# Performance work log

Measured on AMD Instinct MI355X. Metric: run time of the kernel, lower is better.

## Reference

```python
import jax, jax.numpy as jnp
import numpy as np

# Grids: sparse_shape=(41,320,320); after spcv1 stride(2,1,1) pad1 k3 -> (21,320,320);
# after spcv2 stride(2,1,1) pad(0,1,1) k3 -> (10,320,320); after spcv3 k(3,1,1) stride(2,1,1) -> (4,320,320)
GRID0 = (41, 320, 320)
GRID1 = (21, 320, 320)
GRID2 = (10, 320, 320)
GRID3 = (4, 320, 320)
T = 3
C_IN = 16
BN_EPS = 1e-3


def _idx_grid(coords, shape):
    g = -np.ones(shape, np.int32)
    g[coords[:, 0], coords[:, 1], coords[:, 2]] = np.arange(len(coords), dtype=np.int32)
    return g


def _subm_nbrs(coords, grid):
    M = len(coords)
    nbr = -np.ones((M, 27), np.int32)
    sh = np.array(grid.shape)
    k = 0
    for dz in (-1, 0, 1):
        for dy in (-1, 0, 1):
            for dx in (-1, 0, 1):
                c = coords + np.array([dz, dy, dx])
                ok = np.all((c >= 0) & (c < sh), axis=1)
                nbr[ok, k] = grid[c[ok, 0], c[ok, 1], c[ok, 2]]
                k += 1
    return nbr


def _spconv_pairs(coords_in, grid_in, out_shape, ksz, stride, pad):
    ksz = np.array(ksz); st = np.array(stride); pd = np.array(pad); osh = np.array(out_shape)
    cands = []
    for kz in range(ksz[0]):
        for ky in range(ksz[1]):
            for kx in range(ksz[2]):
                o = coords_in + pd - np.array([kz, ky, kx])
                ok = np.all(o % st == 0, axis=1)
                o = o[ok] // st
                ok2 = np.all((o >= 0) & (o < osh), axis=1)
                cands.append(o[ok2])
    coords_out = np.unique(np.concatenate(cands, 0), axis=0)
    M = len(coords_out); K = int(np.prod(ksz))
    idx = -np.ones((M, K), np.int32)
    sh = np.array(grid_in.shape)
    k = 0
    for kz in range(ksz[0]):
        for ky in range(ksz[1]):
            for kx in range(ksz[2]):
                ci = coords_out * st - pd + np.array([kz, ky, kx])
                ok = np.all((ci >= 0) & (ci < sh), axis=1)
                idx[ok, k] = grid_in[ci[ok, 0], ci[ok, 1], ci[ok, 2]]
                k += 1
    return coords_out.astype(np.int32), idx


def setup_inputs() -> dict:
    rng = np.random.default_rng(0)
    # clustered lidar-like active voxels
    nC, nP = 60, 150
    centers = np.stack([rng.uniform(6, 35, nC), rng.uniform(12, 308, nC), rng.uniform(12, 308, nC)], 1)
    pts = centers[:, None, :] + rng.normal(size=(nC, nP, 3)) * np.array([1.2, 2.0, 2.0])
    pts = np.clip(np.round(pts).astype(np.int64).reshape(-1, 3), 0, np.array(GRID0) - 1)
    coords0 = np.unique(pts, axis=0)
    g0 = _idx_grid(coords0, GRID0)
    nbr0 = _subm_nbrs(coords0, g0)
    coords1, idx1 = _spconv_pairs(coords0, g0, GRID1, (3, 3, 3), (2, 1, 1), (1, 1, 1))
    g1 = _idx_grid(coords1, GRID1)
    nbr1 = _subm_nbrs(coords1, g1)
    coords2, idx2 = _spconv_pairs(coords1, g1, GRID2, (3, 3, 3), (2, 1, 1), (0, 1, 1))
    g2 = _idx_grid(coords2, GRID2)
    nbr2 = _subm_nbrs(coords2, g2)
    coords3, idx3 = _spconv_pairs(coords2, g2, GRID3, (3, 1, 1), (2, 1, 1), (0, 0, 0))

    def w(K, ci, co):
        return jnp.asarray(rng.standard_normal((K, ci, co)) / np.sqrt(K * ci), jnp.float32)

    def bn(n, c):
        g = rng.uniform(0.5, 1.5, (n, c)); b = rng.standard_normal((n, c)) * 0.1
        m = rng.standard_normal((n, c)) * 0.1; v = rng.uniform(0.5, 1.5, (n, c))
        return jnp.asarray(np.stack([g, b, m, v], 1), jnp.float32)  # [n,4,c]

    return dict(
        voxel_features=jnp.asarray(rng.standard_normal((T, len(coords0), C_IN)), jnp.float32),
        w_subm1=w(27, 16, 32), w_subm2=w(27, 32, 32), w_spcv1=w(27, 32, 64),
        w_subm3=w(27, 64, 64), w_subm4=w(27, 64, 64), w_subm5=w(27, 64, 64),
        w_spcv2=w(27, 64, 64), w_subm6=w(27, 64, 64), w_subm7=w(27, 64, 64), w_subm8=w(27, 64, 64),
        w_spcv3=w(3, 64, 64),
        w_ad1=jnp.asarray(rng.standard_normal((64, 64)) / 8.0, jnp.float32),
        w_ad2=jnp.asarray(rng.standard_normal((64, 64)) / 8.0, jnp.float32),
        bn32=bn(2, 32), bn64=bn(9, 64), bn_ad=bn(1, 64)[0],
        nbr0=jnp.asarray(nbr0), idx1=jnp.asarray(idx1), nbr1=jnp.asarray(nbr1),
        idx2=jnp.asarray(idx2), nbr2=jnp.asarray(nbr2), idx3=jnp.asarray(idx3),
        coords3=jnp.asarray(coords3))


def _bn_eval(x, p):
    g, b, m, v = p
    return (x - m) * (g * jax.lax.rsqrt(v + BN_EPS)) + b


def _gconv(f, idx, w):
    # gather-GEMM: idx [M,K] (-1 = missing), f [Min,Ci], w [K,Ci,Co]
    g = jnp.where((idx >= 0)[:, :, None], f[jnp.clip(idx, 0)], 0.0)  # [M,K,Ci]
    return jnp.einsum('mki,kio->mo', g, w)


def reference(voxel_features, w_subm1, w_subm2, w_spcv1, w_subm3, w_subm4, w_subm5,
              w_spcv2, w_subm6, w_subm7, w_subm8, w_spcv3, w_ad1, w_ad2,
              bn32, bn64, bn_ad, nbr0, idx1, nbr1, idx2, nbr2, idx3, coords3):
    relu = jax.nn.relu
    s0 = s1 = s2 = None  # cached previous-frame sparse features per level
    outs = []
    for t in range(voxel_features.shape[0]):
        a0 = 0.0 if s0 is None else jnp.mean(s0, 0)
        a1 = 0.0 if s1 is None else jnp.mean(s1, 0)
        a2 = 0.0 if s2 is None else jnp.mean(s2, 0)
        x = relu(_bn_eval(_gconv(voxel_features[t], nbr0, w_subm1), bn32[0]))
        x = relu(_bn_eval(_gconv(x, nbr0, w_subm2), bn32[1]))
        x3 = relu(_bn_eval(_gconv(x, idx1, w_spcv1) + a0, bn64[0])); s0 = x3
        x = relu(_bn_eval(_gconv(x3, nbr1, w_subm3), bn64[1]))
        x = relu(_bn_eval(_gconv(x, nbr1, w_subm4), bn64[2]))
        x6 = relu(_bn_eval(_gconv(x, nbr1, w_subm5), bn64[3]))
        x7 = relu(_bn_eval(_gconv(x6, idx2, w_spcv2) + a1, bn64[4])); s1 = x7
        x = relu(_bn_eval(_gconv(x7, nbr2, w_subm6), bn64[5]))
        x = relu(_bn_eval(_gconv(x, nbr2, w_subm7), bn64[6]))
        x10 = relu(_bn_eval(_gconv(x, nbr2, w_subm8), bn64[7]))
        x11 = relu(_bn_eval(_gconv(x10, idx3, w_spcv3) + a2, bn64[8])); s2 = x11
        dense = jnp.zeros(GRID3 + (64,), x11.dtype).at[coords3[:, 0], coords3[:, 1], coords3[:, 2]].set(x11)
        outs.append(dense.transpose(3, 0, 1, 2).reshape(1, 64 * GRID3[0], GRID3[1], GRID3[2]))
        adapt = lambda s: (relu(_bn_eval(s @ w_ad1, bn_ad)) @ w_ad2) / 10.0
        s0, s1, s2 = adapt(s0), adapt(s1), adapt(s2)
    return jnp.stack(outs)
```

## Files before the change

kernel.cpp:

```cpp
#include <hip/hip_runtime.h>


typedef _Float16 f16;
typedef _Float16 f16x8 __attribute__((ext_vector_type(8)));
typedef float    f32x4 __attribute__((ext_vector_type(4)));

#define BN_EPS_F 1e-3f

__global__ __launch_bounds__(256)
void fill_zero(float4* __restrict__ p, long n4)
{
    long i  = blockIdx.x * 256L + threadIdx.x;
    long st = (long)gridDim.x * 256L;
    float4 z = make_float4(0.f, 0.f, 0.f, 0.f);
    for (; i < n4; i += st) p[i] = z;
}

__global__ __launch_bounds__(256)
void vf_convert(const float* __restrict__ vf, f16* __restrict__ vf16, int nrows)
{
    int i = blockIdx.x * 256 + threadIdx.x;
    if (i >= nrows * 32) return;
    int r = i >> 5, c = i & 31;
    vf16[i] = (c < 16) ? (f16)vf[r * 16 + c] : (f16)0;
}

struct WXA { const float* s; f16* d; int K, Ci, Co, CiD, off; };
struct WXAll { WXA w[11]; };

__global__ __launch_bounds__(256)
void wxform_all(WXAll wa, int total)
{
    int i = blockIdx.x * 256 + threadIdx.x;
    if (i >= total) return;
    int j = 0;
    #pragma unroll
    for (int t = 1; t < 11; ++t) if (i >= wa.w[t].off) j = t;
    const float* s = wa.w[j].s;
    f16* d = wa.w[j].d;
    int Ci = wa.w[j].Ci, Co = wa.w[j].Co, CiD = wa.w[j].CiD;
    int e = i - wa.w[j].off;
    int cc = Co * CiD;
    int k = e / cc; int rem = e - k * cc;
    int co = rem / CiD; int ci = rem - co * CiD;
    float v = (ci < Ci) ? s[((size_t)k * Ci + ci) * Co + co] : 0.f;
    d[e] = (f16)v;
}

template<int Ci, int Co, int K, int ROWS, int KSPLIT, bool SCATTER>
__global__ __launch_bounds__((ROWS/16)*KSPLIT*64)
void gconv(const f16* __restrict__ fin, const int* __restrict__ idx,
           const f16* __restrict__ wT,
           const float* __restrict__ bnp,
           const float* __restrict__ avec,
           f16* __restrict__ fout,
           const int* __restrict__ coords, float* __restrict__ dout,
           int M, int blocksPerFrame, long finStride, long foutStride)
{
    constexpr int RW  = ROWS / 16;
    constexpr int NW  = RW * KSPLIT;
    constexpr int NT  = NW * 64;
    constexpr int NF  = Co / 16;
    constexpr int KK  = Ci / 32;
    constexpr int TPG = (K + KSPLIT - 1) / KSPLIT;
    constexpr int CoP = Co + 4;

    __shared__ int   sIdx[ROWS][K];
    __shared__ float red[KSPLIT > 1 ? KSPLIT - 1 : 1][ROWS][CoP];

    const int tid  = threadIdx.x;
    const int lane = tid & 63;
    const int w    = tid >> 6;
    const int wq   = w % RW;
    const int g    = w / RW;
    const int l15  = lane & 15;
    const int kg   = lane >> 4;

    const int bid   = blockIdx.x;
    const int frame = bid / blocksPerFrame;
    const int fb    = bid - frame * blocksPerFrame;
    const f16* finF = fin + (long)frame * finStride;
    f16* foutF      = fout + (long)frame * foutStride;
    const int m0    = fb * ROWS;

    for (int i = tid; i < ROWS * K; i += NT) {
        int r = i / K, k = i - r * K;
        int m = m0 + r;
        sIdx[r][k] = (m < M) ? idx[(long)m * K + k] : -1;
    }
    __syncthreads();

    f32x4 acc[NF];
    #pragma unroll
    for (int nf = 0; nf < NF; ++nf) acc[nf] = (f32x4){0.f, 0.f, 0.f, 0.f};

    const int arow = wq * 16 + l15;
    const int k0 = g * TPG;

    #pragma unroll
    for (int kt = 0; kt < TPG; ++kt) {
        int k = k0 + kt;
        if (k >= K) break;
        int n = sIdx[arow][k];
        #pragma unroll
        for (int kk = 0; kk < KK; ++kk) {
            f16x8 af = {};
            if (n >= 0)
                af = *(const f16x8*)&finF[(long)n * Ci + kk * 32 + kg * 8];
            #pragma unroll
            for (int nf = 0; nf < NF; ++nf) {
                f16x8 bf = *(const f16x8*)&wT[((long)k * Co + nf * 16 + l15) * Ci + kk * 32 + kg * 8];
                acc[nf] = __builtin_amdgcn_mfma_f32_16x16x32_f16(af, bf, acc[nf], 0, 0, 0);
            }
        }
    }

    if (KSPLIT > 1) {
        if (g > 0) {
            #pragma unroll
            for (int nf = 0; nf < NF; ++nf)
                #pragma unroll
                for (int j = 0; j < 4; ++j)
                    red[g - 1][wq * 16 + kg * 4 + j][nf * 16 + l15] = acc[nf][j];
        }
        __syncthreads();
        if (g == 0) {
            #pragma unroll
            for (int nf = 0; nf < NF; ++nf)
                #pragma unroll
                for (int j = 0; j < 4; ++j)
                    #pragma unroll
                    for (int gi = 0; gi < KSPLIT - 1; ++gi)
                        acc[nf][j] += red[gi][wq * 16 + kg * 4 + j][nf * 16 + l15];
        }
    }

    if (g == 0) {
        #pragma unroll
        for (int nf = 0; nf < NF; ++nf) {
            int c = nf * 16 + l15;
            float gg = bnp[c], bb = bnp[Co + c], mu = bnp[2 * Co + c], vv = bnp[3 * Co + c];
            float sc = gg * rsqrtf(vv + BN_EPS_F);
            float sh = bb - mu * sc;
            float av = avec ? avec[c] : 0.f;
            #pragma unroll
            for (int j = 0; j < 4; ++j) {
                int row = wq * 16 + kg * 4 + j;
                int m = m0 + row;
                if (m < M) {
                    float x = acc[nf][j] + av;
                    float y = fmaxf(fmaf(x, sc, sh), 0.f);
                    foutF[(long)m * Co + c] = (f16)y;
                    if (SCATTER) {
                        int z  = coords[m * 3 + 0];
                        int yy = coords[m * 3 + 1];
                        int xx = coords[m * 3 + 2];
                        dout[(long)(c * 4 + z) * (320 * 320) + yy * 320 + xx] = y;
                    }
                }
            }
        }
    }
}

__global__ __launch_bounds__(64)
void adapt_partial3(const f16* __restrict__ x3, const f16* __restrict__ x7,
                    const f16* __restrict__ x11,
                    const float* __restrict__ w_ad1, const float* __restrict__ bn_ad,
                    float* __restrict__ pb,
                    int M1, int M2, int M3, int g1, int g2)
{
    __shared__ float wl[64 * 64];
    const int c = threadIdx.x;
    for (int i = c; i < 64 * 64; i += 64) wl[i] = w_ad1[i];
    float gg = bn_ad[c], bb = bn_ad[64 + c], mu = bn_ad[128 + c], vv = bn_ad[192 + c];
    float sc = gg * rsqrtf(vv + BN_EPS_F);
    float sh = bb - mu * sc;
    __syncthreads();

    int b = blockIdx.x;
    const f16* s; int M, r0;
    if (b < g1)           { s = x3;  M = M1; r0 = b * 64; }
    else if (b < g1 + g2) { s = x7;  M = M2; r0 = (b - g1) * 64; }
    else                  { s = x11; M = M3; r0 = (b - g1 - g2) * 64; }

    float hacc = 0.f;
    int r1 = min(r0 + 64, M);
    for (int r = r0; r < r1; ++r) {
        float acc = 0.f;
        #pragma unroll
        for (int i8 = 0; i8 < 8; ++i8) {
            f16x8 sv = *(const f16x8*)&s[(size_t)r * 64 + i8 * 8];
            #pragma unroll
            for (int e = 0; e < 8; ++e)
                acc = fmaf((float)sv[e], wl[(i8 * 8 + e) * 64 + c], acc);
        }
        hacc += fmaxf(fmaf(acc, sc, sh), 0.f);
    }
    pb[(size_t)b * 64 + c] = hacc;
}

__global__ __launch_bounds__(192)
void adapt_final3(const float* __restrict__ pb, const float* __restrict__ w_ad2,
                  float* __restrict__ av, int g1, int g2, int g3,
                  float invM1, float invM2, float invM3)
{
    __shared__ float h[3][64];
    const int lvl = threadIdx.x >> 6;
    const int c   = threadIdx.x & 63;
    int base = (lvl == 0) ? 0 : (lvl == 1 ? g1 : g1 + g2);
    int n    = (lvl == 0) ? g1 : (lvl == 1 ? g2 : g3);
    float invM = (lvl == 0) ? invM1 : (lvl == 1 ? invM2 : invM3);
    float acc = 0.f;
    for (int i = 0; i < n; ++i) acc += pb[(size_t)(base + i) * 64 + c];
    h[lvl][c] = acc * invM;
    __syncthreads();
    float o = 0.f;
    #pragma unroll 8
    for (int j = 0; j < 64; ++j) o = fmaf(h[lvl][j], w_ad2[j * 64 + c], o);
    av[lvl * 64 + c] = o * 0.1f;
}

extern "C" void kernel_launch(void* const* d_in, const int* in_sizes, int n_in,
                              void* d_out, int out_size, void* d_ws, size_t ws_size,
                              hipStream_t stream)
{
    const float* vf      = (const float*)d_in[0];
    const float* w_subm1 = (const float*)d_in[1];
    const float* w_subm2 = (const float*)d_in[2];
    const float* w_spcv1 = (const float*)d_in[3];
    const float* w_subm3 = (const float*)d_in[4];
    const float* w_subm4 = (const float*)d_in[5];
    const float* w_subm5 = (const float*)d_in[6];
    const float* w_spcv2 = (const float*)d_in[7];
    const float* w_subm6 = (const float*)d_in[8];
    const float* w_subm7 = (const float*)d_in[9];
    const float* w_subm8 = (const float*)d_in[10];
    const float* w_spcv3 = (const float*)d_in[11];
    const float* w_ad1   = (const float*)d_in[12];
    const float* w_ad2   = (const float*)d_in[13];
    const float* bn32    = (const float*)d_in[14];
    const float* bn64    = (const float*)d_in[15];
    const float* bn_ad   = (const float*)d_in[16];
    const int* nbr0    = (const int*)d_in[17];
    const int* idx1    = (const int*)d_in[18];
    const int* nbr1    = (const int*)d_in[19];
    const int* idx2    = (const int*)d_in[20];
    const int* nbr2    = (const int*)d_in[21];
    const int* idx3    = (const int*)d_in[22];
    const int* coords3 = (const int*)d_in[23];

    const int M0 = in_sizes[0]  / (3 * 16);
    const int M1 = in_sizes[18] / 27;
    const int M2 = in_sizes[20] / 27;
    const int M3 = in_sizes[22] / 3;

    char* base = (char*)d_ws;
    size_t off = 0;
    auto alloc = [&](size_t bytes) -> void* {
        void* p = base + off;
        off = (off + bytes + 255) & ~(size_t)255;
        return p;
    };
    f16* wt1  = (f16*)alloc((size_t)27 * 32 * 32 * 2);
    f16* wt2  = (f16*)alloc((size_t)27 * 32 * 32 * 2);
    f16* wtc1 = (f16*)alloc((size_t)27 * 64 * 32 * 2);
    f16* wt3  = (f16*)alloc((size_t)27 * 64 * 64 * 2);
    f16* wt4  = (f16*)alloc((size_t)27 * 64 * 64 * 2);
    f16* wt5  = (f16*)alloc((size_t)27 * 64 * 64 * 2);
    f16* wtc2 = (f16*)alloc((size_t)27 * 64 * 64 * 2);
    f16* wt6  = (f16*)alloc((size_t)27 * 64 * 64 * 2);
    f16* wt7  = (f16*)alloc((size_t)27 * 64 * 64 * 2);
    f16* wt8  = (f16*)alloc((size_t)27 * 64 * 64 * 2);
    f16* wtc3 = (f16*)alloc((size_t)3  * 64 * 64 * 2);
    f16* vf16  = (f16*)alloc((size_t)3 * M0 * 32 * 2);
    f16* buf0a = (f16*)alloc((size_t)3 * M0 * 32 * 2);
    f16* buf0b = (f16*)alloc((size_t)3 * M0 * 32 * 2);
    f16* x3    = (f16*)alloc((size_t)M1 * 64 * 2);
    f16* buf1a = (f16*)alloc((size_t)M1 * 64 * 2);
    f16* buf1b = (f16*)alloc((size_t)M1 * 64 * 2);
    f16* x7    = (f16*)alloc((size_t)M2 * 64 * 2);
    f16* buf2a = (f16*)alloc((size_t)M2 * 64 * 2);
    f16* buf2b = (f16*)alloc((size_t)M2 * 64 * 2);
    f16* x11   = (f16*)alloc((size_t)M3 * 64 * 2);
    float* av  = (float*)alloc(192 * 4);
    const int g1a = (M1 + 63) / 64, g2a = (M2 + 63) / 64, g3a = (M3 + 63) / 64;
    float* pb  = (float*)alloc((size_t)(g1a + g2a + g3a) * 64 * 4);
    (void)ws_size; (void)n_in;

    WXAll wa;
    int woff = 0;
    auto addw = [&](int slot, const float* s, f16* d, int K, int Ci, int Co, int CiD) {
        wa.w[slot] = {s, d, K, Ci, Co, CiD, woff};
        woff += K * Co * CiD;
    };
    addw(0,  w_subm1, wt1,  27, 16, 32, 32);
    addw(1,  w_subm2, wt2,  27, 32, 32, 32);
    addw(2,  w_spcv1, wtc1, 27, 32, 64, 32);
    addw(3,  w_subm3, wt3,  27, 64, 64, 64);
    addw(4,  w_subm4, wt4,  27, 64, 64, 64);
    addw(5,  w_subm5, wt5,  27, 64, 64, 64);
    addw(6,  w_spcv2, wtc2, 27, 64, 64, 64);
    addw(7,  w_subm6, wt6,  27, 64, 64, 64);
    addw(8,  w_subm7, wt7,  27, 64, 64, 64);
    addw(9,  w_subm8, wt8,  27, 64, 64, 64);
    addw(10, w_spcv3, wtc3, 3,  64, 64, 64);
    wxform_all<<<(woff + 255) / 256, 256, 0, stream>>>(wa, woff);
    vf_convert<<<(3 * M0 * 32 + 255) / 256, 256, 0, stream>>>(vf, vf16, 3 * M0);
    fill_zero<<<2048, 256, 0, stream>>>((float4*)d_out, (long)out_size / 4);

    const int g0w = (M0 + 31) / 32;
    const int g1w = (M1 + 31) / 32;
    const int g2w = (M2 + 31) / 32;
    const int g3w = (M3 + 31) / 32;
    const long s0 = (long)M0 * 32;

    gconv<32,32,27,32,4,false><<<3 * g0w, 512, 0, stream>>>(
        vf16,  nbr0, wt1, bn32,       nullptr, buf0a, nullptr, nullptr, M0, g0w, s0, s0);
    gconv<32,32,27,32,4,false><<<3 * g0w, 512, 0, stream>>>(
        buf0a, nbr0, wt2, bn32 + 128, nullptr, buf0b, nullptr, nullptr, M0, g0w, s0, s0);

    for (int t = 0; t < 3; ++t) {
        const float* a0 = (t == 0) ? nullptr : av + 0;
        const float* a1 = (t == 0) ? nullptr : av + 64;
        const float* a2 = (t == 0) ? nullptr : av + 128;
        float* doutT = (float*)d_out + (size_t)t * 256 * 320 * 320;

        gconv<32,64,27,32,4,false><<<g1w, 512, 0, stream>>>(
            buf0b + (long)t * s0, idx1, wtc1, bn64, a0, x3, nullptr, nullptr, M1, g1w, 0, 0);
        gconv<64,64,27,32,4,false><<<g1w, 512, 0, stream>>>(
            x3,    nbr1, wt3, bn64 + 256,  nullptr, buf1a, nullptr, nullptr, M1, g1w, 0, 0);
        gconv<64,64,27,32,4,false><<<g1w, 512, 0, stream>>>(
            buf1a, nbr1, wt4, bn64 + 512,  nullptr, buf1b, nullptr, nullptr, M1, g1w, 0, 0);
        gconv<64,64,27,32,4,false><<<g1w, 512, 0, stream>>>(
            buf1b, nbr1, wt5, bn64 + 768,  nullptr, buf1a, nullptr, nullptr, M1, g1w, 0, 0);
        gconv<64,64,27,32,4,false><<<g2w, 512, 0, stream>>>(
            buf1a, idx2, wtc2, bn64 + 1024, a1,     x7,    nullptr, nullptr, M2, g2w, 0, 0);
        gconv<64,64,27,32,4,false><<<g2w, 512, 0, stream>>>(
            x7,    nbr2, wt6, bn64 + 1280, nullptr, buf2a, nullptr, nullptr, M2, g2w, 0, 0);
        gconv<64,64,27,32,4,false><<<g2w, 512, 0, stream>>>(
            buf2a, nbr2, wt7, bn64 + 1536, nullptr, buf2b, nullptr, nullptr, M2, g2w, 0, 0);
        gconv<64,64,27,32,4,false><<<g2w, 512, 0, stream>>>(
            buf2b, nbr2, wt8, bn64 + 1792, nullptr, buf2a, nullptr, nullptr, M2, g2w, 0, 0);
        gconv<64,64,3,32,3,true><<<g3w, 384, 0, stream>>>(
            buf2a, idx3, wtc3, bn64 + 2048, a2,    x11,   coords3, doutT,   M3, g3w, 0, 0);

        if (t < 2) {
            adapt_partial3<<<g1a + g2a + g3a, 64, 0, stream>>>(
                x3, x7, x11, w_ad1, bn_ad, pb, M1, M2, M3, g1a, g2a);
            adapt_final3<<<1, 192, 0, stream>>>(
                pb, w_ad2, av, g1a, g2a, g3a, 1.f / M1, 1.f / M2, 1.f / M3);
        }
    }
}
```

Before: 1.674 ms.

## Shrink gconv blocks to 16 rows with per-wave kernel-offset split

Restructures the gather-conv kernel so each block handles 16 output rows. Waves split the padded kernel offsets (27 padded to 28, 3 to 4), each wave taking a fixed number of taps. Neighbor indices are loaded straight into registers instead of staged through shared memory, and the split-K reduction is folded into the epilogue. Weights are zero-padded for the extra tap so the loops need no bounds checks. This doubles the block count, costs extra index loads and weight reads per row, and adds a wasted padded tap.

```diff
diff --git a/kernel.cpp b/kernel.cpp
--- a/kernel.cpp
+++ b/kernel.cpp
@@ -25,7 +25,7 @@
     vf16[i] = (c < 16) ? (f16)vf[r * 16 + c] : (f16)0;
 }
 
-struct WXA { const float* s; f16* d; int K, Ci, Co, CiD, off; };
+struct WXA { const float* s; f16* d; int K, Kp, Ci, Co, CiD, off; };
 struct WXAll { WXA w[11]; };
 
 __global__ __launch_bounds__(256)
@@ -38,17 +38,17 @@
     for (int t = 1; t < 11; ++t) if (i >= wa.w[t].off) j = t;
     const float* s = wa.w[j].s;
     f16* d = wa.w[j].d;
-    int Ci = wa.w[j].Ci, Co = wa.w[j].Co, CiD = wa.w[j].CiD;
+    int K = wa.w[j].K, Ci = wa.w[j].Ci, Co = wa.w[j].Co, CiD = wa.w[j].CiD;
     int e = i - wa.w[j].off;
     int cc = Co * CiD;
     int k = e / cc; int rem = e - k * cc;
     int co = rem / CiD; int ci = rem - co * CiD;
-    float v = (ci < Ci) ? s[((size_t)k * Ci + ci) * Co + co] : 0.f;
+    float v = (k < K && ci < Ci) ? s[((size_t)k * Ci + ci) * Co + co] : 0.f;
     d[e] = (f16)v;
 }
 
-template<int Ci, int Co, int K, int ROWS, int KSPLIT, bool SCATTER>
-__global__ __launch_bounds__((ROWS/16)*KSPLIT*64)
+template<int Ci, int Co, int K, int KPAD, int TPW, bool SCATTER>
+__global__ __launch_bounds__((KPAD/TPW)*64)
 void gconv(const f16* __restrict__ fin, const int* __restrict__ idx,
            const f16* __restrict__ wT,
            const float* __restrict__ bnp,
@@ -57,22 +57,16 @@
            const int* __restrict__ coords, float* __restrict__ dout,
            int M, int blocksPerFrame, long finStride, long foutStride)
 {
-    constexpr int RW  = ROWS / 16;
-    constexpr int NW  = RW * KSPLIT;
-    constexpr int NT  = NW * 64;
+    constexpr int KSPLIT = KPAD / TPW;
     constexpr int NF  = Co / 16;
     constexpr int KK  = Ci / 32;
-    constexpr int TPG = (K + KSPLIT - 1) / KSPLIT;
     constexpr int CoP = Co + 4;
 
-    __shared__ int   sIdx[ROWS][K];
-    __shared__ float red[KSPLIT > 1 ? KSPLIT - 1 : 1][ROWS][CoP];
+    __shared__ float red[KSPLIT - 1][16][CoP];
 
     const int tid  = threadIdx.x;
     const int lane = tid & 63;
-    const int w    = tid >> 6;
-    const int wq   = w % RW;
-    const int g    = w / RW;
+    const int g    = tid >> 6;
     const int l15  = lane & 15;
     const int kg   = lane >> 4;
 
@@ -81,27 +75,26 @@
     const int fb    = bid - frame * blocksPerFrame;
     const f16* finF = fin + (long)frame * finStride;
     f16* foutF      = fout + (long)frame * foutStride;
-    const int m0    = fb * ROWS;
-
-    for (int i = tid; i < ROWS * K; i += NT) {
-        int r = i / K, k = i - r * K;
-        int m = m0 + r;
-        sIdx[r][k] = (m < M) ? idx[(long)m * K + k] : -1;
-    }
-    __syncthreads();
+    const int m0    = fb * 16;
+    const int mrow  = m0 + l15;
+    const bool rowok = mrow < M;
+
+    const int k0 = g * TPW;
+    int nidx[TPW];
+    #pragma unroll
+    for (int kt = 0; kt < TPW; ++kt) {
+        int k = k0 + kt;
+        nidx[kt] = (rowok && k < K) ? idx[(long)mrow * K + k] : -1;
+    }
 
     f32x4 acc[NF];
     #pragma unroll
     for (int nf = 0; nf < NF; ++nf) acc[nf] = (f32x4){0.f, 0.f, 0.f, 0.f};
 
-    const int arow = wq * 16 + l15;
-    const int k0 = g * TPG;
-
     #pragma unroll
-    for (int kt = 0; kt < TPG; ++kt) {
+    for (int kt = 0; kt < TPW; ++kt) {
         int k = k0 + kt;
-        if (k >= K) break;
-        int n = sIdx[arow][k];
+        int n = nidx[kt];
         #pragma unroll
         for (int kk = 0; kk < KK; ++kk) {
             f16x8 af = {};
@@ -115,26 +108,14 @@
         }
     }
 
-    if (KSPLIT > 1) {
-        if (g > 0) {
+    if (g > 0) {
+        #pragma unroll
+        for (int nf = 0; nf < NF; ++nf)
             #pragma unroll
-            for (int nf = 0; nf < NF; ++nf)
-                #pragma unroll
-                for (int j = 0; j < 4; ++j)
-                    red[g - 1][wq * 16 + kg * 4 + j][nf * 16 + l15] = acc[nf][j];
-        }
-        __syncthreads();
-        if (g == 0) {
-            #pragma unroll
-            for (int nf = 0; nf < NF; ++nf)
-                #pragma unroll
-                for (int j = 0; j < 4; ++j)
-                    #pragma unroll
-                    for (int gi = 0; gi < KSPLIT - 1; ++gi)
-                        acc[nf][j] += red[gi][wq * 16 + kg * 4 + j][nf * 16 + l15];
-        }
-    }
-
+            for (int j = 0; j < 4; ++j)
+                red[g - 1][kg * 4 + j][nf * 16 + l15] = acc[nf][j];
+    }
+    __syncthreads();
     if (g == 0) {
         #pragma unroll
         for (int nf = 0; nf < NF; ++nf) {
@@ -145,10 +126,13 @@
             float av = avec ? avec[c] : 0.f;
             #pragma unroll
             for (int j = 0; j < 4; ++j) {
-                int row = wq * 16 + kg * 4 + j;
+                int row = kg * 4 + j;
                 int m = m0 + row;
                 if (m < M) {
                     float x = acc[nf][j] + av;
+                    #pragma unroll
+                    for (int gi = 0; gi < KSPLIT - 1; ++gi)
+                        x += red[gi][row][c];
                     float y = fmaxf(fmaf(x, sc, sh), 0.f);
                     foutF[(long)m * Co + c] = (f16)y;
                     if (SCATTER) {
@@ -262,17 +246,17 @@
         off = (off + bytes + 255) & ~(size_t)255;
         return p;
     };
-    f16* wt1  = (f16*)alloc((size_t)27 * 32 * 32 * 2);
-    f16* wt2  = (f16*)alloc((size_t)27 * 32 * 32 * 2);
-    f16* wtc1 = (f16*)alloc((size_t)27 * 64 * 32 * 2);
-    f16* wt3  = (f16*)alloc((size_t)27 * 64 * 64 * 2);
-    f16* wt4  = (f16*)alloc((size_t)27 * 64 * 64 * 2);
-    f16* wt5  = (f16*)alloc((size_t)27 * 64 * 64 * 2);
-    f16* wtc2 = (f16*)alloc((size_t)27 * 64 * 64 * 2);
-    f16* wt6  = (f16*)alloc((size_t)27 * 64 * 64 * 2);
-    f16* wt7  = (f16*)alloc((size_t)27 * 64 * 64 * 2);
-    f16* wt8  = (f16*)alloc((size_t)27 * 64 * 64 * 2);
-    f16* wtc3 = (f16*)alloc((size_t)3  * 64 * 64 * 2);
+    f16* wt1  = (f16*)alloc((size_t)28 * 32 * 32 * 2);
+    f16* wt2  = (f16*)alloc((size_t)28 * 32 * 32 * 2);
+    f16* wtc1 = (f16*)alloc((size_t)28 * 64 * 32 * 2);
+    f16* wt3  = (f16*)alloc((size_t)28 * 64 * 64 * 2);
+    f16* wt4  = (f16*)alloc((size_t)28 * 64 * 64 * 2);
+    f16* wt5  = (f16*)alloc((size_t)28 * 64 * 64 * 2);
+    f16* wtc2 = (f16*)alloc((size_t)28 * 64 * 64 * 2);
+    f16* wt6  = (f16*)alloc((size_t)28 * 64 * 64 * 2);
+    f16* wt7  = (f16*)alloc((size_t)28 * 64 * 64 * 2);
+    f16* wt8  = (f16*)alloc((size_t)28 * 64 * 64 * 2);
+    f16* wtc3 = (f16*)alloc((size_t)4  * 64 * 64 * 2);
     f16* vf16  = (f16*)alloc((size_t)3 * M0 * 32 * 2);
     f16* buf0a = (f16*)alloc((size_t)3 * M0 * 32 * 2);
     f16* buf0b = (f16*)alloc((size_t)3 * M0 * 32 * 2);
@@ -290,34 +274,34 @@
 
     WXAll wa;
     int woff = 0;
-    auto addw = [&](int slot, const float* s, f16* d, int K, int Ci, int Co, int CiD) {
-        wa.w[slot] = {s, d, K, Ci, Co, CiD, woff};
-        woff += K * Co * CiD;
+    auto addw = [&](int slot, const float* s, f16* d, int K, int Kp, int Ci, int Co, int CiD) {
+        wa.w[slot] = {s, d, K, Kp, Ci, Co, CiD, woff};
+        woff += Kp * Co * CiD;
     };
-    addw(0,  w_subm1, wt1,  27, 16, 32, 32);
-    addw(1,  w_subm2, wt2,  27, 32, 32, 32);
-    addw(2,  w_spcv1, wtc1, 27, 32, 64, 32);
-    addw(3,  w_subm3, wt3,  27, 64, 64, 64);
-    addw(4,  w_subm4, wt4,  27, 64, 64, 64);
-    addw(5,  w_subm5, wt5,  27, 64, 64, 64);
-    addw(6,  w_spcv2, wtc2, 27, 64, 64, 64);
-    addw(7,  w_subm6, wt6,  27, 64, 64, 64);
-    addw(8,  w_subm7, wt7,  27, 64, 64, 64);
-    addw(9,  w_subm8, wt8,  27, 64, 64, 64);
-    addw(10, w_spcv3, wtc3, 3,  64, 64, 64);
+    addw(0,  w_subm1, wt1,  27, 28, 16, 32, 32);
+    addw(1,  w_subm2, wt2,  27, 28, 32, 32, 32);
+    addw(2,  w_spcv1, wtc1, 27, 28, 32, 64, 32);
+    addw(3,  w_subm3, wt3,  27, 28, 64, 64, 64);
+    addw(4,  w_subm4, wt4,  27, 28, 64, 64, 64);
+    addw(5,  w_subm5, wt5,  27, 28, 64, 64, 64);
+    addw(6,  w_spcv2, wtc2, 27, 28, 64, 64, 64);
+    addw(7,  w_subm6, wt6,  27, 28, 64, 64, 64);
+    addw(8,  w_subm7, wt7,  27, 28, 64, 64, 64);
+    addw(9,  w_subm8, wt8,  27, 28, 64, 64, 64);
+    addw(10, w_spcv3, wtc3, 3,  4,  64, 64, 64);
     wxform_all<<<(woff + 255) / 256, 256, 0, stream>>>(wa, woff);
     vf_convert<<<(3 * M0 * 32 + 255) / 256, 256, 0, stream>>>(vf, vf16, 3 * M0);
     fill_zero<<<2048, 256, 0, stream>>>((float4*)d_out, (long)out_size / 4);
 
-    const int g0w = (M0 + 31) / 32;
-    const int g1w = (M1 + 31) / 32;
-    const int g2w = (M2 + 31) / 32;
-    const int g3w = (M3 + 31) / 32;
+    const int g0w = (M0 + 15) / 16;
+    const int g1w = (M1 + 15) / 16;
+    const int g2w = (M2 + 15) / 16;
+    const int g3w = (M3 + 15) / 16;
     const long s0 = (long)M0 * 32;
 
-    gconv<32,32,27,32,4,false><<<3 * g0w, 512, 0, stream>>>(
+    gconv<32,32,27,28,4,false><<<3 * g0w, 448, 0, stream>>>(
         vf16,  nbr0, wt1, bn32,       nullptr, buf0a, nullptr, nullptr, M0, g0w, s0, s0);
-    gconv<32,32,27,32,4,false><<<3 * g0w, 512, 0, stream>>>(
+    gconv<32,32,27,28,4,false><<<3 * g0w, 448, 0, stream>>>(
         buf0a, nbr0, wt2, bn32 + 128, nullptr, buf0b, nullptr, nullptr, M0, g0w, s0, s0);
 
     for (int t = 0; t < 3; ++t) {
@@ -326,23 +310,23 @@
         const float* a2 = (t == 0) ? nullptr : av + 128;
         float* doutT = (float*)d_out + (size_t)t * 256 * 320 * 320;
 
-        gconv<32,64,27,32,4,false><<<g1w, 512, 0, stream>>>(
+        gconv<32,64,27,28,4,false><<<g1w, 448, 0, stream>>>(
             buf0b + (long)t * s0, idx1, wtc1, bn64, a0, x3, nullptr, nullptr, M1, g1w, 0, 0);
-        gconv<64,64,27,32,4,false><<<g1w, 512, 0, stream>>>(
+        gconv<64,64,27,28,4,false><<<g1w, 448, 0, stream>>>(
             x3,    nbr1, wt3, bn64 + 256,  nullptr, buf1a, nullptr, nullptr, M1, g1w, 0, 0);
-        gconv<64,64,27,32,4,false><<<g1w, 512, 0, stream>>>(
+        gconv<64,64,27,28,4,false><<<g1w, 448, 0, stream>>>(
             buf1a, nbr1, wt4, bn64 + 512,  nullptr, buf1b, nullptr, nullptr, M1, g1w, 0, 0);
-        gconv<64,64,27,32,4,false><<<g1w, 512, 0, stream>>>(
+        gconv<64,64,27,28,4,false><<<g1w, 448, 0, stream>>>(
             buf1b, nbr1, wt5, bn64 + 768,  nullptr, buf1a, nullptr, nullptr, M1, g1w, 0, 0);
-        gconv<64,64,27,32,4,false><<<g2w, 512, 0, stream>>>(
+        gconv<64,64,27,28,4,false><<<g2w, 448, 0, stream>>>(
             buf1a, idx2, wtc2, bn64 + 1024, a1,     x7,    nullptr, nullptr, M2, g2w, 0, 0);
-        gconv<64,64,27,32,4,false><<<g2w, 512, 0, stream>>>(
+        gconv<64,64,27,28,4,false><<<g2w, 448, 0, stream>>>(
             x7,    nbr2, wt6, bn64 + 1280, nullptr, buf2a, nullptr, nullptr, M2, g2w, 0, 0);
-        gconv<64,64,27,32,4,false><<<g2w, 512, 0, stream>>>(
+        gconv<64,64,27,28,4,false><<<g2w, 448, 0, stream>>>(
             buf2a, nbr2, wt7, bn64 + 1536, nullptr, buf2b, nullptr, nullptr, M2, g2w, 0, 0);
-        gconv<64,64,27,32,4,false><<<g2w, 512, 0, stream>>>(
+        gconv<64,64,27,28,4,false><<<g2w, 448, 0, stream>>>(
             buf2b, nbr2, wt8, bn64 + 1792, nullptr, buf2a, nullptr, nullptr, M2, g2w, 0, 0);
-        gconv<64,64,3,32,3,true><<<g3w, 384, 0, stream>>>(
+        gconv<64,64,3,4,1,true><<<g3w, 256, 0, stream>>>(
             buf2a, idx3, wtc3, bn64 + 2048, a2,    x11,   coords3, doutT,   M3, g3w, 0, 0);
 
         if (t < 2) {
```

Measured after the change: 1.779 ms. 6.3% more time.

## Stage per-offset weights in double-buffered LDS and prefetch gathered rows across kernel offsets

Applied to the files above, without the earlier changes.

Drops the split across kernel offsets and its shared-memory reduction. Each 256-thread block now handles 64 output rows and walks all kernel offsets in sequence. Weights for the next offset are loaded into registers and written into a double-buffered, padded LDS tile, and the gathered input rows for the next offset are prefetched while the MFMAs for the current one run. This is meant to cut redundant global weight reads and hide gather latency. The cost is one barrier per offset, a serial K loop, and fewer blocks, which lowers parallelism on the smaller layers.

```diff
diff --git a/kernel.cpp b/kernel.cpp
--- a/kernel.cpp
+++ b/kernel.cpp
@@ -47,8 +47,8 @@
     d[e] = (f16)v;
 }
 
-template<int Ci, int Co, int K, int ROWS, int KSPLIT, bool SCATTER>
-__global__ __launch_bounds__((ROWS/16)*KSPLIT*64)
+template<int Ci, int Co, int K, bool SCATTER>
+__global__ __launch_bounds__(256)
 void gconv(const f16* __restrict__ fin, const int* __restrict__ idx,
            const f16* __restrict__ wT,
            const float* __restrict__ bnp,
@@ -57,22 +57,19 @@
            const int* __restrict__ coords, float* __restrict__ dout,
            int M, int blocksPerFrame, long finStride, long foutStride)
 {
-    constexpr int RW  = ROWS / 16;
-    constexpr int NW  = RW * KSPLIT;
-    constexpr int NT  = NW * 64;
     constexpr int NF  = Co / 16;
     constexpr int KK  = Ci / 32;
-    constexpr int TPG = (K + KSPLIT - 1) / KSPLIT;
-    constexpr int CoP = Co + 4;
-
-    __shared__ int   sIdx[ROWS][K];
-    __shared__ float red[KSPLIT > 1 ? KSPLIT - 1 : 1][ROWS][CoP];
+    constexpr int CiP = Ci + 8;
+    constexpr int cpr = Ci / 8;
+    constexpr int CH  = Co * cpr;
+    constexpr int NLD = (CH + 255) / 256;
+
+    __shared__ f16 Bw[2][Co * CiP];
+    __shared__ int sIdx[64][K];
 
     const int tid  = threadIdx.x;
     const int lane = tid & 63;
-    const int w    = tid >> 6;
-    const int wq   = w % RW;
-    const int g    = w / RW;
+    const int wq   = tid >> 6;
     const int l15  = lane & 15;
     const int kg   = lane >> 4;
 
@@ -81,82 +78,103 @@
     const int fb    = bid - frame * blocksPerFrame;
     const f16* finF = fin + (long)frame * finStride;
     f16* foutF      = fout + (long)frame * foutStride;
-    const int m0    = fb * ROWS;
-
-    for (int i = tid; i < ROWS * K; i += NT) {
+    const int m0    = fb * 64;
+
+    for (int i = tid; i < 64 * K; i += 256) {
         int r = i / K, k = i - r * K;
         int m = m0 + r;
         sIdx[r][k] = (m < M) ? idx[(long)m * K + k] : -1;
     }
+    for (int i = tid; i < CH; i += 256) {
+        int co = i / cpr, q = i - co * cpr;
+        *(uint4*)&Bw[0][co * CiP + q * 8] = *(const uint4*)&wT[(long)co * Ci + q * 8];
+    }
     __syncthreads();
+
+    const int arow = wq * 16 + l15;
+
+    f16x8 afc[KK];
+    {
+        int n = sIdx[arow][0];
+        #pragma unroll
+        for (int kk = 0; kk < KK; ++kk) {
+            f16x8 v = {};
+            if (n >= 0) v = *(const f16x8*)&finF[(long)n * Ci + kk * 32 + kg * 8];
+            afc[kk] = v;
+        }
+    }
 
     f32x4 acc[NF];
     #pragma unroll
     for (int nf = 0; nf < NF; ++nf) acc[nf] = (f32x4){0.f, 0.f, 0.f, 0.f};
 
-    const int arow = wq * 16 + l15;
-    const int k0 = g * TPG;
+    #pragma unroll 1
+    for (int k = 0; k < K; ++k) {
+        const bool more = (k + 1 < K);
+        uint4 wreg[NLD];
+        if (more) {
+            #pragma unroll
+            for (int u = 0; u < NLD; ++u) {
+                int i = tid + u * 256;
+                if (i < CH) {
+                    int co = i / cpr, q = i - co * cpr;
+                    wreg[u] = *(const uint4*)&wT[((long)(k + 1) * Co + co) * Ci + q * 8];
+                }
+            }
+        }
+        f16x8 afn[KK];
+        {
+            int n = more ? sIdx[arow][k + 1] : -1;
+            #pragma unroll
+            for (int kk = 0; kk < KK; ++kk) {
+                f16x8 v = {};
+                if (n >= 0) v = *(const f16x8*)&finF[(long)n * Ci + kk * 32 + kg * 8];
+                afn[kk] = v;
+            }
+        }
+        const f16* bwb = &Bw[k & 1][0];
+        #pragma unroll
+        for (int kk = 0; kk < KK; ++kk) {
+            #pragma unroll
+            for (int nf = 0; nf < NF; ++nf) {
+                f16x8 bf = *(const f16x8*)&bwb[(nf * 16 + l15) * CiP + kk * 32 + kg * 8];
+                acc[nf] = __builtin_amdgcn_mfma_f32_16x16x32_f16(afc[kk], bf, acc[nf], 0, 0, 0);
+            }
+        }
+        if (more) {
+            #pragma unroll
+            for (int u = 0; u < NLD; ++u) {
+                int i = tid + u * 256;
+                if (i < CH) {
+                    int co = i / cpr, q = i - co * cpr;
+                    *(uint4*)&Bw[(k + 1) & 1][co * CiP + q * 8] = wreg[u];
+                }
+            }
+            __syncthreads();
+        }
+        #pragma unroll
+        for (int kk = 0; kk < KK; ++kk) afc[kk] = afn[kk];
+    }
 
     #pragma unroll
-    for (int kt = 0; kt < TPG; ++kt) {
-        int k = k0 + kt;
-        if (k >= K) break;
-        int n = sIdx[arow][k];
-        #pragma unroll
-        for (int kk = 0; kk < KK; ++kk) {
-            f16x8 af = {};
-            if (n >= 0)
-                af = *(const f16x8*)&finF[(long)n * Ci + kk * 32 + kg * 8];
-            #pragma unroll
-            for (int nf = 0; nf < NF; ++nf) {
-                f16x8 bf = *(const f16x8*)&wT[((long)k * Co + nf * 16 + l15) * Ci + kk * 32 + kg * 8];
-                acc[nf] = __builtin_amdgcn_mfma_f32_16x16x32_f16(af, bf, acc[nf], 0, 0, 0);
-            }
-        }
-    }
-
-    if (KSPLIT > 1) {
-        if (g > 0) {
-            #pragma unroll
-            for (int nf = 0; nf < NF; ++nf)
-                #pragma unroll
-                for (int j = 0; j < 4; ++j)
-                    red[g - 1][wq * 16 + kg * 4 + j][nf * 16 + l15] = acc[nf][j];
-        }
-        __syncthreads();
-        if (g == 0) {
-            #pragma unroll
-            for (int nf = 0; nf < NF; ++nf)
-                #pragma unroll
-                for (int j = 0; j < 4; ++j)
-                    #pragma unroll
-                    for (int gi = 0; gi < KSPLIT - 1; ++gi)
-                        acc[nf][j] += red[gi][wq * 16 + kg * 4 + j][nf * 16 + l15];
-        }
-    }
-
-    if (g == 0) {
-        #pragma unroll
-        for (int nf = 0; nf < NF; ++nf) {
-            int c = nf * 16 + l15;
-            float gg = bnp[c], bb = bnp[Co + c], mu = bnp[2 * Co + c], vv = bnp[3 * Co + c];
-            float sc = gg * rsqrtf(vv + BN_EPS_F);
-            float sh = bb - mu * sc;
-            float av = avec ? avec[c] : 0.f;
-            #pragma unroll
-            for (int j = 0; j < 4; ++j) {
-                int row = wq * 16 + kg * 4 + j;
-                int m = m0 + row;
-                if (m < M) {
-                    float x = acc[nf][j] + av;
-                    float y = fmaxf(fmaf(x, sc, sh), 0.f);
-                    foutF[(long)m * Co + c] = (f16)y;
-                    if (SCATTER) {
-                        int z  = coords[m * 3 + 0];
-                        int yy = coords[m * 3 + 1];
-                        int xx = coords[m * 3 + 2];
-                        dout[(long)(c * 4 + z) * (320 * 320) + yy * 320 + xx] = y;
-                    }
+    for (int nf = 0; nf < NF; ++nf) {
+        int c = nf * 16 + l15;
+        float gg = bnp[c], bb = bnp[Co + c], mu = bnp[2 * Co + c], vv = bnp[3 * Co + c];
+        float sc = gg * rsqrtf(vv + BN_EPS_F);
+        float sh = bb - mu * sc;
+        float av = avec ? avec[c] : 0.f;
+        #pragma unroll
+        for (int j = 0; j < 4; ++j) {
+            int m = m0 + wq * 16 + kg * 4 + j;
+            if (m < M) {
+                float x = acc[nf][j] + av;
+                float y = fmaxf(fmaf(x, sc, sh), 0.f);
+                foutF[(long)m * Co + c] = (f16)y;
+                if (SCATTER) {
+                    int z  = coords[m * 3 + 0];
+                    int yy = coords[m * 3 + 1];
+                    int xx = coords[m * 3 + 2];
+                    dout[(long)(c * 4 + z) * (320 * 320) + yy * 320 + xx] = y;
                 }
             }
         }
@@ -309,16 +327,16 @@
     vf_convert<<<(3 * M0 * 32 + 255) / 256, 256, 0, stream>>>(vf, vf16, 3 * M0);
     fill_zero<<<2048, 256, 0, stream>>>((float4*)d_out, (long)out_size / 4);
 
-    const int g0w = (M0 + 31) / 32;
-    const int g1w = (M1 + 31) / 32;
-    const int g2w = (M2 + 31) / 32;
-    const int g3w = (M3 + 31) / 32;
+    const int g0 = (M0 + 63) / 64;
+    const int g1 = (M1 + 63) / 64;
+    const int g2 = (M2 + 63) / 64;
+    const int g3 = (M3 + 63) / 64;
     const long s0 = (long)M0 * 32;
 
-    gconv<32,32,27,32,4,false><<<3 * g0w, 512, 0, stream>>>(
-        vf16,  nbr0, wt1, bn32,       nullptr, buf0a, nullptr, nullptr, M0, g0w, s0, s0);
-    gconv<32,32,27,32,4,false><<<3 * g0w, 512, 0, stream>>>(
-        buf0a, nbr0, wt2, bn32 + 128, nullptr, buf0b, nullptr, nullptr, M0, g0w, s0, s0);
+    gconv<32,32,27,false><<<3 * g0, 256, 0, stream>>>(
+        vf16,  nbr0, wt1, bn32,       nullptr, buf0a, nullptr, nullptr, M0, g0, s0, s0);
+    gconv<32,32,27,false><<<3 * g0, 256, 0, stream>>>(
+        buf0a, nbr0, wt2, bn32 + 128, nullptr, buf0b, nullptr, nullptr, M0, g0, s0, s0);
 
     for (int t = 0; t < 3; ++t) {
         const float* a0 = (t == 0) ? nullptr : av + 0;
@@ -326,24 +344,24 @@
         const float* a2 = (t == 0) ? nullptr : av + 128;
         float* doutT = (float*)d_out + (size_t)t * 256 * 320 * 320;
 
-        gconv<32,64,27,32,4,false><<<g1w, 512, 0, stream>>>(
-            buf0b + (long)t * s0, idx1, wtc1, bn64, a0, x3, nullptr, nullptr, M1, g1w, 0, 0);
-        gconv<64,64,27,32,4,false><<<g1w, 512, 0, stream>>>(
-            x3,    nbr1, wt3, bn64 + 256,  nullptr, buf1a, nullptr, nullptr, M1, g1w, 0, 0);
-        gconv<64,64,27,32,4,false><<<g1w, 512, 0, stream>>>(
-            buf1a, nbr1, wt4, bn64 + 512,  nullptr, buf1b, nullptr, nullptr, M1, g1w, 0, 0);
-        gconv<64,64,27,32,4,false><<<g1w, 512, 0, stream>>>(
-            buf1b, nbr1, wt5, bn64 + 768,  nullptr, buf1a, nullptr, nullptr, M1, g1w, 0, 0);
-        gconv<64,64,27,32,4,false><<<g2w, 512, 0, stream>>>(
-            buf1a, idx2, wtc2, bn64 + 1024, a1,     x7,    nullptr, nullptr, M2, g2w, 0, 0);
-        gconv<64,64,27,32,4,false><<<g2w, 512, 0, stream>>>(
-            x7,    nbr2, wt6, bn64 + 1280, nullptr, buf2a, nullptr, nullptr, M2, g2w, 0, 0);
-        gconv<64,64,27,32,4,false><<<g2w, 512, 0, stream>>>(
-            buf2a, nbr2, wt7, bn64 + 1536, nullptr, buf2b, nullptr, nullptr, M2, g2w, 0, 0);
-        gconv<64,64,27,32,4,false><<<g2w, 512, 0, stream>>>(
-            buf2b, nbr2, wt8, bn64 + 1792, nullptr, buf2a, nullptr, nullptr, M2, g2w, 0, 0);
-        gconv<64,64,3,32,3,true><<<g3w, 384, 0, stream>>>(
-            buf2a, idx3, wtc3, bn64 + 2048, a2,    x11,   coords3, doutT,   M3, g3w, 0, 0);
+        gconv<32,64,27,false><<<g1, 256, 0, stream>>>(
+            buf0b + (long)t * s0, idx1, wtc1, bn64, a0, x3, nullptr, nullptr, M1, g1, 0, 0);
+        gconv<64,64,27,false><<<g1, 256, 0, stream>>>(
+            x3,    nbr1, wt3, bn64 + 256,  nullptr, buf1a, nullptr, nullptr, M1, g1, 0, 0);
+        gconv<64,64,27,false><<<g1, 256, 0, stream>>>(
+            buf1a, nbr1, wt4, bn64 + 512,  nullptr, buf1b, nullptr, nullptr, M1, g1, 0, 0);
+        gconv<64,64,27,false><<<g1, 256, 0, stream>>>(
+            buf1b, nbr1, wt5, bn64 + 768,  nullptr, buf1a, nullptr, nullptr, M1, g1, 0, 0);
+        gconv<64,64,27,false><<<g2, 256, 0, stream>>>(
+            buf1a, idx2, wtc2, bn64 + 1024, a1,     x7,    nullptr, nullptr, M2, g2, 0, 0);
+        gconv<64,64,27,false><<<g2, 256, 0, stream>>>(
+            x7,    nbr2, wt6, bn64 + 1280, nullptr, buf2a, nullptr, nullptr, M2, g2, 0, 0);
+        gconv<64,64,27,false><<<g2, 256, 0, stream>>>(
+            buf2a, nbr2, wt7, bn64 + 1536, nullptr, buf2b, nullptr, nullptr, M2, g2, 0, 0);
+        gconv<64,64,27,false><<<g2, 256, 0, stream>>>(
+            buf2b, nbr2, wt8, bn64 + 1792, nullptr, buf2a, nullptr, nullptr, M2, g2, 0, 0);
+        gconv<64,64,3,true><<<g3, 256, 0, stream>>>(
+            buf2a, idx3, wtc3, bn64 + 2048, a2,    x11,   coords3, doutT,   M3, g3, 0, 0);
 
         if (t < 2) {
             adapt_partial3<<<g1a + g2a + g3a, 64, 0, stream>>>(
```

Measured after the change: 1.532 ms. -8.5%, faster.
